# Performance work log

Measured on AMD Instinct MI355X. Metric: run time of the kernel, lower is better.

The kernel has to match this reference:

```python
import jax, jax.numpy as jnp
import numpy as np

H = 256
NF = 513


def gru(x_seq, wih, whh, bih, bhh):
    """PyTorch-semantics single-layer GRU, batch_first. x_seq: [B,T,D] -> [B,T,H]."""
    B = x_seq.shape[0]
    # precompute input projections once: [B,T,3H] -> time-major [T,B,3H]
    xproj = jnp.einsum('btd,gd->btg', x_seq, wih) + bih
    xproj = jnp.swapaxes(xproj, 0, 1)
    h0 = jnp.zeros((B, H), dtype=x_seq.dtype)

    def step(h, xp):
        hp = h @ whh.T + bhh
        xr, xz, xn = jnp.split(xp, 3, axis=-1)
        hr, hz, hn = jnp.split(hp, 3, axis=-1)
        r = jax.nn.sigmoid(xr + hr)
        z = jax.nn.sigmoid(xz + hz)
        n = jnp.tanh(xn + r * hn)
        h_new = (1.0 - z) * n + z * h
        return h_new, h_new

    _, hs = jax.lax.scan(step, h0, xproj)
    return jnp.swapaxes(hs, 0, 1)  # [B,T,H]


def setup_inputs() -> dict:
    key = jax.random.key(0)
    ks = jax.random.split(key, 20)
    s = 0.05

    def gru_params(i):
        return (
            jax.random.normal(ks[i], (3 * H, H), jnp.float32) * s,
            jax.random.normal(ks[i + 1], (3 * H, H), jnp.float32) * s,
            jax.random.normal(ks[i + 2], (3 * H,), jnp.float32) * s,
            jax.random.normal(ks[i + 3], (3 * H,), jnp.float32) * s,
        )

    x = jax.random.normal(ks[0], (32, 2, 1000, NF), jnp.float32)
    ds_w = jax.random.normal(ks[1], (H, 2 * NF), jnp.float32) * s
    ds_b = jax.random.normal(ks[2], (H,), jnp.float32) * s
    g1 = gru_params(3)
    gr = gru_params(7)
    gi = gru_params(11)
    dr_w = jax.random.normal(ks[15], (NF, H), jnp.float32) * s
    dr_b = jax.random.normal(ks[16], (NF,), jnp.float32) * s
    di_w = jax.random.normal(ks[17], (NF, H), jnp.float32) * s
    di_b = jax.random.normal(ks[18], (NF,), jnp.float32) * s
    return {
        'x': x, 'ds_w': ds_w, 'ds_b': ds_b,
        'g1_wih': g1[0], 'g1_whh': g1[1], 'g1_bih': g1[2], 'g1_bhh': g1[3],
        'gr_wih': gr[0], 'gr_whh': gr[1], 'gr_bih': gr[2], 'gr_bhh': gr[3],
        'gi_wih': gi[0], 'gi_whh': gi[1], 'gi_bih': gi[2], 'gi_bhh': gi[3],
        'dr_w': dr_w, 'dr_b': dr_b, 'di_w': di_w, 'di_b': di_b,
    }


def reference(x, ds_w, ds_b,
              g1_wih, g1_whh, g1_bih, g1_bhh,
              gr_wih, gr_whh, gr_bih, gr_bhh,
              gi_wih, gi_whh, gi_bih, gi_bhh,
              dr_w, dr_b, di_w, di_b):
    real_mag = x[:, 0, :, :]   # [B,T,513]
    imag_mag = x[:, 1, :, :]
    shared_in = jnp.concatenate([real_mag, imag_mag], axis=2)  # [B,T,1026]
    shared_out = shared_in @ ds_w.T + ds_b                     # [B,T,256]
    shared_gru = gru(shared_out, g1_wih, g1_whh, g1_bih, g1_bhh)
    real_1 = gru(shared_gru, gr_wih, gr_whh, gr_bih, gr_bhh)
    real_o = real_1 @ dr_w.T + dr_b
    imag_1 = gru(shared_gru, gi_wih, gi_whh, gi_bih, gi_bhh)
    imag_o = imag_1 @ di_w.T + di_b
    return (real_o[:, None, :, :], imag_o[:, None, :, :])
```

## Files before the change

kernel.cpp:

```cpp
#include <hip/hip_runtime.h>
#include <cstdint>
#include <cstddef>

#define NB   32
#define NT   1000
#define NF   513
#define NH   256
#define NG   768
#define NM   (NB*NT)

#define XP_ELEMS  ((size_t)NM * NG)
#define H_ELEMS   ((size_t)NM * NH)
#define WPK_ELEMS ((size_t)NG * NH / 2)
#define OUT_HALF  ((size_t)NM * NF)

typedef _Float16 f16x2 __attribute__((ext_vector_type(2)));

static __device__ __forceinline__ f16x2 as_f16x2(float x) {
    return __builtin_bit_cast(f16x2, x);
}
static __device__ __forceinline__ f16x2 as_f16x2u(unsigned x) {
    return __builtin_bit_cast(f16x2, x);
}

#if __has_builtin(__builtin_amdgcn_fdot2)
static __device__ __forceinline__ float fdot2(f16x2 h, f16x2 w, float acc) {
    return __builtin_amdgcn_fdot2(h, w, acc, false);
}
#else
static __device__ __forceinline__ float fdot2(f16x2 h, f16x2 w, float acc) {
    return acc + (float)h.x * (float)w.x + (float)h.y * (float)w.y;
}
#endif

#define GEMM_BM 128
#define GEMM_BN 64
#define GEMM_BK 16

template<bool CONCAT>
__global__ __launch_bounds__(256) void gemm_bias_kernel(
    const float* __restrict__ A, const float* __restrict__ W,
    const float* __restrict__ bias, float* __restrict__ C,
    int M, int N, int K)
{
    __shared__ float As[GEMM_BK][GEMM_BM];
    __shared__ float Bs[GEMM_BK][GEMM_BN];
    const int tid = threadIdx.x;
    const int bm = blockIdx.x * GEMM_BM;
    const int bn = blockIdx.y * GEMM_BN;
    const int mt = tid >> 4;
    const int nt = tid & 15;
    const int m0 = mt * 8;
    const int n0 = nt * 4;

    float acc[8][4];
    #pragma unroll
    for (int i = 0; i < 8; ++i)
        #pragma unroll
        for (int j = 0; j < 4; ++j) acc[i][j] = 0.f;

    const bool kvec = ((K & 3) == 0);

    for (int k0 = 0; k0 < K; k0 += GEMM_BK) {
        #pragma unroll
        for (int i = 0; i < 2; ++i) {
            int qid = tid * 2 + i;
            int m   = qid >> 2;
            int kq  = (qid & 3) << 2;
            int gm  = bm + m;
            int gk  = k0 + kq;
            float v0 = 0.f, v1 = 0.f, v2 = 0.f, v3 = 0.f;
            if (gm < M) {
                if (!CONCAT) {
                    if (kvec && gk + 4 <= K) {
                        float4 v = *(const float4*)(A + (size_t)gm * K + gk);
                        v0 = v.x; v1 = v.y; v2 = v.z; v3 = v.w;
                    } else {
                        if (gk + 0 < K) v0 = A[(size_t)gm * K + gk + 0];
                        if (gk + 1 < K) v1 = A[(size_t)gm * K + gk + 1];
                        if (gk + 2 < K) v2 = A[(size_t)gm * K + gk + 2];
                        if (gk + 3 < K) v3 = A[(size_t)gm * K + gk + 3];
                    }
                } else {
                    int b = gm / NT;
                    int t = gm - b * NT;
                    float tmp[4];
                    #pragma unroll
                    for (int u = 0; u < 4; ++u) {
                        int f = gk + u;
                        float val = 0.f;
                        if (f < K) {
                            int ch = (f >= NF) ? 1 : 0;
                            int ff = f - ch * NF;
                            val = A[(((size_t)(b * 2 + ch)) * NT + t) * NF + ff];
                        }
                        tmp[u] = val;
                    }
                    v0 = tmp[0]; v1 = tmp[1]; v2 = tmp[2]; v3 = tmp[3];
                }
            }
            As[kq + 0][m] = v0; As[kq + 1][m] = v1;
            As[kq + 2][m] = v2; As[kq + 3][m] = v3;
        }
        {
            int n  = tid >> 2;
            int kq = (tid & 3) << 2;
            int gn = bn + n;
            int gk = k0 + kq;
            float v0 = 0.f, v1 = 0.f, v2 = 0.f, v3 = 0.f;
            if (gn < N) {
                if (kvec && gk + 4 <= K) {
                    float4 v = *(const float4*)(W + (size_t)gn * K + gk);
                    v0 = v.x; v1 = v.y; v2 = v.z; v3 = v.w;
                } else {
                    if (gk + 0 < K) v0 = W[(size_t)gn * K + gk + 0];
                    if (gk + 1 < K) v1 = W[(size_t)gn * K + gk + 1];
                    if (gk + 2 < K) v2 = W[(size_t)gn * K + gk + 2];
                    if (gk + 3 < K) v3 = W[(size_t)gn * K + gk + 3];
                }
            }
            Bs[kq + 0][n] = v0; Bs[kq + 1][n] = v1;
            Bs[kq + 2][n] = v2; Bs[kq + 3][n] = v3;
        }
        __syncthreads();
        #pragma unroll
        for (int k = 0; k < GEMM_BK; ++k) {
            float a[8], bb[4];
            *(float4*)&a[0] = *(const float4*)&As[k][m0];
            *(float4*)&a[4] = *(const float4*)&As[k][m0 + 4];
            *(float4*)&bb[0] = *(const float4*)&Bs[k][n0];
            #pragma unroll
            for (int i = 0; i < 8; ++i)
                #pragma unroll
                for (int j = 0; j < 4; ++j)
                    acc[i][j] = fmaf(a[i], bb[j], acc[i][j]);
        }
        __syncthreads();
    }
    #pragma unroll
    for (int i = 0; i < 8; ++i) {
        int gm = bm + m0 + i;
        if (gm >= M) continue;
        #pragma unroll
        for (int j = 0; j < 4; ++j) {
            int gn = bn + n0 + j;
            if (gn < N) C[(size_t)gm * N + gn] = acc[i][j] + bias[gn];
        }
    }
}

__global__ __launch_bounds__(256) void pack_whh_f16(
    const float* __restrict__ whh, unsigned* __restrict__ wpk)
{
    int idx = blockIdx.x * 256 + threadIdx.x;
    int k2  = idx / NG;
    int row = idx - k2 * NG;
    float lo = whh[row * NH + 2 * k2];
    float hi = whh[row * NH + 2 * k2 + 1];
    f16x2 w;
    w.x = (_Float16)lo;
    w.y = (_Float16)hi;
    wpk[((size_t)(k2 >> 2) * NG + row) * 4 + (k2 & 3)] = __builtin_bit_cast(unsigned, w);
}

__global__ __launch_bounds__(512, 2) void gru_rec_kernel(
    const float* __restrict__ xpA, const unsigned* __restrict__ wpkA,
    const float* __restrict__ bhhA, float* __restrict__ outA,
    const float* __restrict__ xpB, const unsigned* __restrict__ wpkB,
    const float* __restrict__ bhhB, float* __restrict__ outB,
    int nBatch)
{
    const int wg = blockIdx.x;
    const float* xp;  const unsigned* wpk;  const float* bhh;  float* out;  int b;
    if (wg < nBatch) { xp = xpA; wpk = wpkA; bhh = bhhA; out = outA; b = wg; }
    else             { xp = xpB; wpk = wpkB; bhh = bhhB; out = outB; b = wg - nBatch; }

    const int tid = threadIdx.x;
    const int u   = tid & (NH - 1);
    const int ph  = tid >> 8;

    unsigned w0[64], w1[64], w2[64];
    {
        const uint4* wq4 = (const uint4*)wpk;
        #pragma unroll
        for (int i = 0; i < 16; ++i) {
            const int k2g = ph * 16 + i;
            uint4 a = wq4[(size_t)k2g * NG + u];
            uint4 c = wq4[(size_t)k2g * NG + NH + u];
            uint4 d = wq4[(size_t)k2g * NG + 2 * NH + u];
            w0[4*i+0] = a.x; w0[4*i+1] = a.y; w0[4*i+2] = a.z; w0[4*i+3] = a.w;
            w1[4*i+0] = c.x; w1[4*i+1] = c.y; w1[4*i+2] = c.z; w1[4*i+3] = c.w;
            w2[4*i+0] = d.x; w2[4*i+1] = d.y; w2[4*i+2] = d.z; w2[4*i+3] = d.w;
        }
    }
    float br = 0.f, bz = 0.f, bn = 0.f;
    if (!ph) { br = bhh[u]; bz = bhh[NH + u]; bn = bhh[2 * NH + u]; }

    __shared__ __align__(16) _Float16 hbuf[NH];
    __shared__ float part[3][NH];
    if (tid < NH) hbuf[tid] = (_Float16)0.f;
    float hreg = 0.f;
    __syncthreads();

    float xr = 0.f, xz = 0.f, xn = 0.f;
    if (!ph) {
        const size_t base = (size_t)b * NT * NG + u;
        xr = xp[base];
        xz = xp[base + NH];
        xn = xp[base + 2 * NH];
    }

    for (int t = 0; t < NT; ++t) {
        float pxr = 0.f, pxz = 0.f, pxn = 0.f;
        if (!ph) {
            const int tn = (t + 1 < NT) ? (t + 1) : t;
            const size_t base = ((size_t)b * NT + tn) * NG + u;
            pxr = xp[base];
            pxz = xp[base + NH];
            pxn = xp[base + 2 * NH];
        }

        const float4* h4 = (const float4*)hbuf + ph * 16;
        float a0 = 0.f, a1 = 0.f, c0 = 0.f, c1 = 0.f, d0 = 0.f, d1 = 0.f;
        #pragma unroll
        for (int i = 0; i < 16; ++i) {
            float4 hb = h4[i];
            f16x2 h0 = as_f16x2(hb.x);
            f16x2 h1 = as_f16x2(hb.y);
            f16x2 h2 = as_f16x2(hb.z);
            f16x2 h3 = as_f16x2(hb.w);
            a0 = fdot2(h0, as_f16x2u(w0[4*i+0]), a0);
            a1 = fdot2(h1, as_f16x2u(w0[4*i+1]), a1);
            a0 = fdot2(h2, as_f16x2u(w0[4*i+2]), a0);
            a1 = fdot2(h3, as_f16x2u(w0[4*i+3]), a1);
            c0 = fdot2(h0, as_f16x2u(w1[4*i+0]), c0);
            c1 = fdot2(h1, as_f16x2u(w1[4*i+1]), c1);
            c0 = fdot2(h2, as_f16x2u(w1[4*i+2]), c0);
            c1 = fdot2(h3, as_f16x2u(w1[4*i+3]), c1);
            d0 = fdot2(h0, as_f16x2u(w2[4*i+0]), d0);
            d1 = fdot2(h1, as_f16x2u(w2[4*i+1]), d1);
            d0 = fdot2(h2, as_f16x2u(w2[4*i+2]), d0);
            d1 = fdot2(h3, as_f16x2u(w2[4*i+3]), d1);
        }
        const float sr = a0 + a1;
        const float sz = c0 + c1;
        const float sn = d0 + d1;

        if (ph) { part[0][u] = sr; part[1][u] = sz; part[2][u] = sn; }
        __syncthreads();

        if (!ph) {
            const float hr = sr + part[0][u] + br;
            const float hz = sz + part[1][u] + bz;
            const float hn = sn + part[2][u] + bn;
            const float r    = 1.f / (1.f + __expf(-(xr + hr)));
            const float z    = 1.f / (1.f + __expf(-(xz + hz)));
            const float pre  = xn + r * hn;
            const float e2   = __expf(2.f * pre);
            const float n    = 1.f - 2.f / (e2 + 1.f);
            const float hnew = (1.f - z) * n + z * hreg;
            hreg = hnew;
            hbuf[u] = (_Float16)hnew;
            out[((size_t)b * NT + t) * NH + u] = hnew;
        }
        __syncthreads();

        xr = pxr; xz = pxz; xn = pxn;
    }
}

extern "C" void kernel_launch(void* const* d_in, const int* in_sizes, int n_in,
                              void* d_out, int out_size, void* d_ws, size_t ws_size,
                              hipStream_t stream)
{
    const float* x      = (const float*)d_in[0];
    const float* ds_w   = (const float*)d_in[1];
    const float* ds_b   = (const float*)d_in[2];
    const float* g1_wih = (const float*)d_in[3];
    const float* g1_whh = (const float*)d_in[4];
    const float* g1_bih = (const float*)d_in[5];
    const float* g1_bhh = (const float*)d_in[6];
    const float* gr_wih = (const float*)d_in[7];
    const float* gr_whh = (const float*)d_in[8];
    const float* gr_bih = (const float*)d_in[9];
    const float* gr_bhh = (const float*)d_in[10];
    const float* gi_wih = (const float*)d_in[11];
    const float* gi_whh = (const float*)d_in[12];
    const float* gi_bih = (const float*)d_in[13];
    const float* gi_bhh = (const float*)d_in[14];
    const float* dr_w   = (const float*)d_in[15];
    const float* dr_b   = (const float*)d_in[16];
    const float* di_w   = (const float*)d_in[17];
    const float* di_b   = (const float*)d_in[18];

    float* out = (float*)d_out;
    float* ws  = (float*)d_ws;

    unsigned* wpk1 = (unsigned*)ws;
    unsigned* wpkr = wpk1 + WPK_ELEMS;
    unsigned* wpki = wpkr + WPK_ELEMS;
    float* xpA = ws + 3 * WPK_ELEMS;

    const size_t need_conc = (3 * WPK_ELEMS + 2 * XP_ELEMS + 3 * H_ELEMS) * sizeof(float);
    const bool conc = ws_size >= need_conc;

    float *xpB, *so, *sg, *r1, *i1;
    if (conc) {
        xpB = xpA + XP_ELEMS;
        so  = xpB + XP_ELEMS;
        sg  = so + H_ELEMS;
        i1  = sg + H_ELEMS;
        r1  = so;
    } else {
        xpB = xpA;
        so  = xpA + XP_ELEMS;
        sg  = so + H_ELEMS;
        r1  = so;
        i1  = so;
    }

    const dim3 blk(256);
    const dim3 rblk(512);
    const dim3 gN256(NM / GEMM_BM, NH / GEMM_BN);
    const dim3 gN768(NM / GEMM_BM, NG / GEMM_BN);
    const dim3 gN513(NM / GEMM_BM, (NF + GEMM_BN - 1) / GEMM_BN);
    const dim3 gPack((NG * NH / 2) / 256);

    pack_whh_f16<<<gPack, blk, 0, stream>>>(g1_whh, wpk1);
    pack_whh_f16<<<gPack, blk, 0, stream>>>(gr_whh, wpkr);
    pack_whh_f16<<<gPack, blk, 0, stream>>>(gi_whh, wpki);

    gemm_bias_kernel<true><<<gN256, blk, 0, stream>>>(x, ds_w, ds_b, so, NM, NH, 2 * NF);
    gemm_bias_kernel<false><<<gN768, blk, 0, stream>>>(so, g1_wih, g1_bih, xpA, NM, NG, NH);
    gru_rec_kernel<<<dim3(NB), rblk, 0, stream>>>(
        xpA, wpk1, g1_bhh, sg, xpA, wpk1, g1_bhh, sg, NB);

    if (conc) {
        gemm_bias_kernel<false><<<gN768, blk, 0, stream>>>(sg, gr_wih, gr_bih, xpA, NM, NG, NH);
        gemm_bias_kernel<false><<<gN768, blk, 0, stream>>>(sg, gi_wih, gi_bih, xpB, NM, NG, NH);
        gru_rec_kernel<<<dim3(2 * NB), rblk, 0, stream>>>(
            xpA, wpkr, gr_bhh, r1, xpB, wpki, gi_bhh, i1, NB);
        gemm_bias_kernel<false><<<gN513, blk, 0, stream>>>(r1, dr_w, dr_b, out, NM, NF, NH);
        gemm_bias_kernel<false><<<gN513, blk, 0, stream>>>(i1, di_w, di_b, out + OUT_HALF, NM, NF, NH);
    } else {
        gemm_bias_kernel<false><<<gN768, blk, 0, stream>>>(sg, gr_wih, gr_bih, xpA, NM, NG, NH);
        gru_rec_kernel<<<dim3(NB), rblk, 0, stream>>>(
            xpA, wpkr, gr_bhh, r1, xpA, wpkr, gr_bhh, r1, NB);
        gemm_bias_kernel<false><<<gN513, blk, 0, stream>>>(r1, dr_w, dr_b, out, NM, NF, NH);
        gemm_bias_kernel<false><<<gN768, blk, 0, stream>>>(sg, gi_wih, gi_bih, xpA, NM, NG, NH);
        gru_rec_kernel<<<dim3(NB), rblk, 0, stream>>>(
            xpA, wpki, gi_bhh, i1, xpA, wpki, gi_bhh, i1, NB);
        gemm_bias_kernel<false><<<gN513, blk, 0, stream>>>(i1, di_w, di_b, out + OUT_HALF, NM, NF, NH);
    }
}
```

Baseline: 3.715 ms.

## Split GRU recurrent matvec so each thread owns one gate row

The recurrent kernel now uses 768 threads per block, one per gate row. Each thread holds that row's full K-slice of packed fp16 weights (128 registers) instead of three gate rows over half of K (192 registers). The x-projection load is spread across all threads, and the gate pre-activations are exchanged through shared memory before the first 256 threads compute the GRU update. The aim is to lower per-thread register pressure and the length of the per-step serial dot-product chain, at the cost of more waves per block and a changed launch-bounds occupancy hint.

```diff
diff --git a/kernel.cpp b/kernel.cpp
--- a/kernel.cpp
+++ b/kernel.cpp
@@ -163,7 +163,7 @@
     wpk[((size_t)(k2 >> 2) * NG + row) * 4 + (k2 & 3)] = __builtin_bit_cast(unsigned, w);
 }
 
-__global__ __launch_bounds__(512, 2) void gru_rec_kernel(
+__global__ __launch_bounds__(768, 3) void gru_rec_kernel(
     const float* __restrict__ xpA, const unsigned* __restrict__ wpkA,
     const float* __restrict__ bhhA, float* __restrict__ outA,
     const float* __restrict__ xpB, const unsigned* __restrict__ wpkB,
@@ -175,87 +175,58 @@
     if (wg < nBatch) { xp = xpA; wpk = wpkA; bhh = bhhA; out = outA; b = wg; }
     else             { xp = xpB; wpk = wpkB; bhh = bhhB; out = outB; b = wg - nBatch; }
 
-    const int tid = threadIdx.x;
-    const int u   = tid & (NH - 1);
-    const int ph  = tid >> 8;
-
-    unsigned w0[64], w1[64], w2[64];
+    const int g  = threadIdx.x;
+    const int u  = g & (NH - 1);
+    const int gi = g >> 8;
+
+    unsigned w[128];
     {
         const uint4* wq4 = (const uint4*)wpk;
         #pragma unroll
-        for (int i = 0; i < 16; ++i) {
-            const int k2g = ph * 16 + i;
-            uint4 a = wq4[(size_t)k2g * NG + u];
-            uint4 c = wq4[(size_t)k2g * NG + NH + u];
-            uint4 d = wq4[(size_t)k2g * NG + 2 * NH + u];
-            w0[4*i+0] = a.x; w0[4*i+1] = a.y; w0[4*i+2] = a.z; w0[4*i+3] = a.w;
-            w1[4*i+0] = c.x; w1[4*i+1] = c.y; w1[4*i+2] = c.z; w1[4*i+3] = c.w;
-            w2[4*i+0] = d.x; w2[4*i+1] = d.y; w2[4*i+2] = d.z; w2[4*i+3] = d.w;
-        }
-    }
-    float br = 0.f, bz = 0.f, bn = 0.f;
-    if (!ph) { br = bhh[u]; bz = bhh[NH + u]; bn = bhh[2 * NH + u]; }
+        for (int i = 0; i < 32; ++i) {
+            uint4 q = wq4[(size_t)i * NG + g];
+            w[4*i+0] = q.x; w[4*i+1] = q.y; w[4*i+2] = q.z; w[4*i+3] = q.w;
+        }
+    }
+    const float bias = bhh[g];
 
     __shared__ __align__(16) _Float16 hbuf[NH];
-    __shared__ float part[3][NH];
-    if (tid < NH) hbuf[tid] = (_Float16)0.f;
+    __shared__ float psum[3][NH];
+    if (g < NH) hbuf[g] = (_Float16)0.f;
     float hreg = 0.f;
     __syncthreads();
 
-    float xr = 0.f, xz = 0.f, xn = 0.f;
-    if (!ph) {
-        const size_t base = (size_t)b * NT * NG + u;
-        xr = xp[base];
-        xz = xp[base + NH];
-        xn = xp[base + 2 * NH];
-    }
+    const size_t xbase = (size_t)b * NT * NG + g;
+    float xv = xp[xbase];
 
     for (int t = 0; t < NT; ++t) {
-        float pxr = 0.f, pxz = 0.f, pxn = 0.f;
-        if (!ph) {
-            const int tn = (t + 1 < NT) ? (t + 1) : t;
-            const size_t base = ((size_t)b * NT + tn) * NG + u;
-            pxr = xp[base];
-            pxz = xp[base + NH];
-            pxn = xp[base + 2 * NH];
-        }
-
-        const float4* h4 = (const float4*)hbuf + ph * 16;
-        float a0 = 0.f, a1 = 0.f, c0 = 0.f, c1 = 0.f, d0 = 0.f, d1 = 0.f;
-        #pragma unroll
-        for (int i = 0; i < 16; ++i) {
+        const int tn = (t + 1 < NT) ? (t + 1) : t;
+        const float xnext = xp[xbase + (size_t)tn * NG];
+
+        const float4* h4 = (const float4*)hbuf;
+        float a0 = 0.f, a1 = 0.f, a2 = 0.f, a3 = 0.f;
+        #pragma unroll
+        for (int i = 0; i < 32; ++i) {
             float4 hb = h4[i];
-            f16x2 h0 = as_f16x2(hb.x);
-            f16x2 h1 = as_f16x2(hb.y);
-            f16x2 h2 = as_f16x2(hb.z);
-            f16x2 h3 = as_f16x2(hb.w);
-            a0 = fdot2(h0, as_f16x2u(w0[4*i+0]), a0);
-            a1 = fdot2(h1, as_f16x2u(w0[4*i+1]), a1);
-            a0 = fdot2(h2, as_f16x2u(w0[4*i+2]), a0);
-            a1 = fdot2(h3, as_f16x2u(w0[4*i+3]), a1);
-            c0 = fdot2(h0, as_f16x2u(w1[4*i+0]), c0);
-            c1 = fdot2(h1, as_f16x2u(w1[4*i+1]), c1);
-            c0 = fdot2(h2, as_f16x2u(w1[4*i+2]), c0);
-            c1 = fdot2(h3, as_f16x2u(w1[4*i+3]), c1);
-            d0 = fdot2(h0, as_f16x2u(w2[4*i+0]), d0);
-            d1 = fdot2(h1, as_f16x2u(w2[4*i+1]), d1);
-            d0 = fdot2(h2, as_f16x2u(w2[4*i+2]), d0);
-            d1 = fdot2(h3, as_f16x2u(w2[4*i+3]), d1);
-        }
-        const float sr = a0 + a1;
-        const float sz = c0 + c1;
-        const float sn = d0 + d1;
-
-        if (ph) { part[0][u] = sr; part[1][u] = sz; part[2][u] = sn; }
+            a0 = fdot2(as_f16x2(hb.x), as_f16x2u(w[4*i+0]), a0);
+            a1 = fdot2(as_f16x2(hb.y), as_f16x2u(w[4*i+1]), a1);
+            a2 = fdot2(as_f16x2(hb.z), as_f16x2u(w[4*i+2]), a2);
+            a3 = fdot2(as_f16x2(hb.w), as_f16x2u(w[4*i+3]), a3);
+        }
+        const float s = ((a0 + a1) + (a2 + a3)) + bias;
+
+        if (gi == 1) {
+            psum[0][u] = s + xv;
+        } else if (gi == 2) {
+            psum[1][u] = s;
+            psum[2][u] = xv;
+        }
         __syncthreads();
 
-        if (!ph) {
-            const float hr = sr + part[0][u] + br;
-            const float hz = sz + part[1][u] + bz;
-            const float hn = sn + part[2][u] + bn;
-            const float r    = 1.f / (1.f + __expf(-(xr + hr)));
-            const float z    = 1.f / (1.f + __expf(-(xz + hz)));
-            const float pre  = xn + r * hn;
+        if (gi == 0) {
+            const float z    = 1.f / (1.f + __expf(-psum[0][u]));
+            const float r    = 1.f / (1.f + __expf(-(xv + s)));
+            const float pre  = psum[2][u] + r * psum[1][u];
             const float e2   = __expf(2.f * pre);
             const float n    = 1.f - 2.f / (e2 + 1.f);
             const float hnew = (1.f - z) * n + z * hreg;
@@ -265,7 +236,7 @@
         }
         __syncthreads();
 
-        xr = pxr; xz = pxz; xn = pxn;
+        xv = xnext;
     }
 }
 
@@ -320,7 +291,7 @@
     }
 
     const dim3 blk(256);
-    const dim3 rblk(512);
+    const dim3 rblk(768);
     const dim3 gN256(NM / GEMM_BM, NH / GEMM_BN);
     const dim3 gN768(NM / GEMM_BM, NG / GEMM_BN);
     const dim3 gN513(NM / GEMM_BM, (NF + GEMM_BN - 1) / GEMM_BN);
```

After: 3.996 ms. +7.6%, slower.
